# Performance work log

Measured on AMD Instinct MI355X. Metric: run time of the kernel, lower is better.

The kernel has to match this reference:

```python
import jax, jax.numpy as jnp
import numpy as np

BLOCK_SIZE = 64
NUM_STEPS = 3
# pad_type='post', init_type='ones', attention_mask=None


def setup_inputs() -> dict:
    key = jax.random.key(0)
    k1, k2, k3 = jax.random.split(key, 3)
    B, H, S, D = 4, 16, 4096, 64
    return {
        "query": jax.random.normal(k1, (B, H, S, D), dtype=jnp.float32),
        "key": jax.random.normal(k2, (B, H, S, D), dtype=jnp.float32),
        "value": jax.random.normal(k3, (B, H, S, D), dtype=jnp.float32),
    }


def _soba_monarch(query, key, value):
    B, H, S, D = query.shape
    bs = BLOCK_SIZE
    nb = -(-S // bs)                 # ceil(S / bs)
    pad = nb * bs - S                # post padding amount
    q = query / (D ** 0.5)

    pad_cfg = ((0, 0), (0, 0), (0, pad), (0, 0))
    Qb = jnp.pad(q, pad_cfg).reshape(B, H, nb, bs, D)      # (l j) v -> l j v
    Kb = jnp.pad(key, pad_cfg).reshape(B, H, nb, bs, D)    # (k i) v -> k i v

    # validity of positions in the padded sequence (post-pad)
    pos_valid = (jnp.arange(nb * bs) < S).reshape(nb, bs)  # [block, within]
    # left factor shape (..., j, l, k): rows of the flattened (l j) axis
    left_mask = jnp.broadcast_to(pos_valid.T[:, :, None], (bs, nb, nb))      # j l k
    # right factor shape (..., k, j, i): columns of the flattened (k i) axis
    right_mask = jnp.broadcast_to(pos_valid[:, None, :], (nb, bs, bs))       # k j i

    NEG = jnp.finfo(q.dtype).min
    # init_type = 'ones'
    left = jnp.broadcast_to(
        jnp.where(left_mask, 1.0 / nb, 0.0), (B, H, bs, nb, nb)
    ).astype(q.dtype)

    for _ in range(NUM_STEPS):
        # beta[k,j,i] = sum_{l,v} left[j,l,k] Q[l,j,v] K[k,i,v]
        beta = jnp.einsum('bhjlk,bhljv,bhkiv->bhkji', left, Qb, Kb, optimize=True)
        tau = jnp.swapaxes(jnp.sum(left, axis=-2), -1, -2)[..., None]        # bhkj1
        tau_zero = jnp.isclose(tau, 0.0)
        tau_safe = jnp.where(tau_zero, 1.0, tau)
        logits_r = jnp.where(right_mask & ~tau_zero, beta / tau_safe, NEG)
        right = jax.nn.softmax(logits_r, axis=-1)
        right = jnp.where(right_mask, right, 0.0)

        # alpha[j,1,k] = sum_i right[k,j,i] log right[k,j,i]  (xlogy)
        r_safe = jnp.where(right > 0, right, 1.0)
        alpha = jnp.sum(right * jnp.log(r_safe), axis=-1)                    # bhkj
        alpha = jnp.swapaxes(alpha, -1, -2)[..., None, :]                    # bhj1k

        beta2 = jnp.einsum('bhkji,bhljv,bhkiv->bhjlk', right, Qb, Kb, optimize=True)
        left = jax.nn.softmax(jnp.where(left_mask, beta2 - alpha, NEG), axis=-1)
        left = jnp.where(left_mask, left, 0.0)

    # multiply: z = L (R V)
    Vb = jnp.pad(value, pad_cfg).reshape(B, H, nb, bs, D)                    # k i v
    Y = jnp.einsum('bhkji,bhkiv->bhkjv', right, Vb)
    Z = jnp.einsum('bhjlk,bhkjv->bhljv', left, Y)
    z = Z.reshape(B, H, nb * bs, D)
    return z[..., :S, :]


def reference(query, key, value):
    return _soba_monarch(query, key, value)
```

## Files before the change

kernel.cpp:

```cpp
#include <hip/hip_runtime.h>


namespace {

typedef __attribute__((ext_vector_type(8))) short short8v;
typedef __attribute__((ext_vector_type(4))) float f32x4;

constexpr int HEADS = 64;
constexpr size_t HEADQ = 262144;
constexpr size_t MATF  = (size_t)HEADS * 262144;

#define MFMA(ACC, A, B) ACC = __builtin_amdgcn_mfma_f32_16x16x32_bf16(A, B, ACC, 0, 0, 0)
#define LD8(arr, row, g8) (*(const short8v*)((arr) + (row) * 72 + (g8) * 8))

__device__ __forceinline__ float rmax16(float m) {
    m = fmaxf(m, __shfl_xor(m, 1));
    m = fmaxf(m, __shfl_xor(m, 2));
    m = fmaxf(m, __shfl_xor(m, 4));
    m = fmaxf(m, __shfl_xor(m, 8));
    return m;
}
__device__ __forceinline__ float rsum16(float s) {
    s += __shfl_xor(s, 1);
    s += __shfl_xor(s, 2);
    s += __shfl_xor(s, 4);
    s += __shfl_xor(s, 8);
    return s;
}

__device__ __forceinline__ void bfsplit(float x, ushort& h, ushort& l) {
    uint u = __float_as_uint(x);
    uint hi = (u + 0x7FFFu + ((u >> 16) & 1u)) & 0xFFFF0000u;
    h = (ushort)(hi >> 16);
    l = (ushort)(__float_as_uint(x - __uint_as_float(hi)) >> 16);
}
__device__ __forceinline__ uint packbf(float x) {
    uint u = __float_as_uint(x);
    uint hi = (u + 0x7FFFu + ((u >> 16) & 1u)) & 0xFFFF0000u;
    return hi | (__float_as_uint(x - __uint_as_float(hi)) >> 16);
}

struct Frag16 { short8v h0, h1, l0, l1; };

__device__ __forceinline__ Frag16 load_packed16(const uint* p) {
    Frag16 f;
    #pragma unroll
    for (int q = 0; q < 4; ++q) {
        uint4 a = *(const uint4*)(p + 4 * q);
        uint vv[4] = {a.x, a.y, a.z, a.w};
        #pragma unroll
        for (int e = 0; e < 4; ++e) {
            const int i = 4 * q + e;
            const ushort hh = (ushort)(vv[e] >> 16), ll = (ushort)(vv[e] & 0xFFFFu);
            if (i < 8) { f.h0[i] = (short)hh; f.l0[i] = (short)ll; }
            else       { f.h1[i - 8] = (short)hh; f.l1[i - 8] = (short)ll; }
        }
    }
    return f;
}
__device__ __forceinline__ Frag16 load_f32x16(const float* p, float s) {
    Frag16 f;
    #pragma unroll
    for (int q = 0; q < 4; ++q) {
        float4 a = *(const float4*)(p + 4 * q);
        float vv[4] = {a.x * s, a.y * s, a.z * s, a.w * s};
        #pragma unroll
        for (int e = 0; e < 4; ++e) {
            const int i = 4 * q + e;
            ushort hh, ll; bfsplit(vv[e], hh, ll);
            if (i < 8) { f.h0[i] = (short)hh; f.l0[i] = (short)ll; }
            else       { f.h1[i - 8] = (short)hh; f.l1[i - 8] = (short)ll; }
        }
    }
    return f;
}
__device__ __forceinline__ void store_rows(ushort* H, ushort* L, int r, int c0,
                                           const Frag16& f) {
    *(short8v*)(H + r * 72 + c0)     = f.h0;
    *(short8v*)(H + r * 72 + c0 + 8) = f.h1;
    *(short8v*)(L + r * 72 + c0)     = f.l0;
    *(short8v*)(L + r * 72 + c0 + 8) = f.l1;
}
__device__ __forceinline__ void scatter_tr(ushort* H, ushort* L, int r, int c0,
                                           const Frag16& f) {
    #pragma unroll
    for (int e = 0; e < 8; ++e) {
        H[(c0 + e) * 72 + r] = (ushort)f.h0[e];
        L[(c0 + e) * 72 + r] = (ushort)f.l0[e];
    }
    #pragma unroll
    for (int e = 0; e < 8; ++e) {
        H[(c0 + 8 + e) * 72 + r] = (ushort)f.h1[e];
        L[(c0 + 8 + e) * 72 + r] = (ushort)f.l1[e];
    }
}

__device__ __forceinline__ void flush_u32(const uint* OS, uint* g, int tid) {
    #pragma unroll
    for (int q = 0; q < 4; ++q) {
        const int off = tid * 4 + q * 1024;
        uint4 v = *(const uint4*)(OS + (off >> 6) * 68 + (off & 63));
        *(uint4*)(g + off) = v;
    }
}

__device__ __forceinline__ void mmstep(const ushort* AH, const ushort* AL,
                                       const ushort* BH, const ushort* BL,
                                       int w, int lo4, int hi4, f32x4 acc[4]) {
    #pragma unroll
    for (int ks = 0; ks < 2; ++ks) {
        short8v ah = LD8(AH, 16 * w + lo4, hi4 + 4 * ks);
        short8v al = LD8(AL, 16 * w + lo4, hi4 + 4 * ks);
        #pragma unroll
        for (int t = 0; t < 4; ++t) {
            short8v bh = LD8(BH, 16 * t + lo4, hi4 + 4 * ks);
            short8v bl = LD8(BL, 16 * t + lo4, hi4 + 4 * ks);
            MFMA(acc[t], ah, bh); MFMA(acc[t], ah, bl); MFMA(acc[t], al, bh);
        }
    }
}

__global__ void kmean_kernel(const float* __restrict__ Q, uint* __restrict__ M) {
    const int wg = blockIdx.x;
    const int h  = wg >> 6, j = wg & 63;
    const int v  = threadIdx.x;
    const float* base = Q + (size_t)h * HEADQ + (size_t)j * 64 + v;
    float acc = 0.f;
    #pragma unroll
    for (int l = 0; l < 64; ++l) acc += base[(size_t)l * 4096];
    M[(size_t)wg * 64 + v] = packbf(acc * (1.0f / 512.0f));
}

template<int FIRST, int LAST>
__global__ __launch_bounds__(256) void bc_kernel(
    const uint*  __restrict__ Gsrc,
    const float* __restrict__ Kmat,
    const float* __restrict__ Vmat,
    const float* __restrict__ tauIn,
    uint*  __restrict__ HmOut,
    float* __restrict__ alphaOut,
    uint*  __restrict__ Yout)
{
    __shared__ uint SM[9216];
    ushort* Ah = (ushort*)SM;        ushort* Al = Ah + 4608;
    ushort* Bh = (ushort*)(SM + 4608); ushort* Bl = Bh + 4608;
    uint* OS  = SM + 4608;
    uint* OS2 = SM;

    const int wg = blockIdx.x, h = wg >> 6, k = wg & 63;
    const int tid = threadIdx.x, r = tid & 63, c0 = (tid >> 6) << 4;

    {
        const uint* gp = FIRST ? (Gsrc + ((size_t)h * 64 + r) * 64 + c0)
                               : (Gsrc + ((size_t)h * 64 + r) * 4096 + (size_t)k * 64 + c0);
        Frag16 fg = load_packed16(gp);
        store_rows(Ah, Al, r, c0, fg);
    }
    Frag16 fk = load_f32x16(Kmat + (size_t)h * HEADQ + (size_t)k * 4096 + r * 64 + c0, 1.f);
    store_rows(Bh, Bl, r, c0, fk);
    Frag16 fv;
    if (LAST)
        fv = load_f32x16(Vmat + (size_t)h * HEADQ + (size_t)k * 4096 + r * 64 + c0, 1.f);

    const int w = tid >> 6, lo4 = tid & 15, hi4 = (tid >> 4) & 3;
    float tvv[4];
    #pragma unroll
    for (int rr = 0; rr < 4; ++rr)
        tvv[rr] = FIRST ? 1.f : tauIn[((size_t)h * 64 + k) * 64 + 16 * w + 4 * hi4 + rr];
    __syncthreads();

    f32x4 acc[4] = {};
    mmstep(Ah, Al, Bh, Bl, w, lo4, hi4, acc);
    __syncthreads();

    #pragma unroll
    for (int rr = 0; rr < 4; ++rr) {
        const int j = 16 * w + 4 * hi4 + rr;
        const bool tz = !(tvv[rr] > 1e-8f);
        const float tvi = tz ? 1.f : 1.f / tvv[rr];
        float lg[4];
        #pragma unroll
        for (int t = 0; t < 4; ++t) lg[t] = acc[t][rr] * tvi;
        float m = rmax16(fmaxf(fmaxf(lg[0], lg[1]), fmaxf(lg[2], lg[3])));
        float e[4], s = 0.f;
        #pragma unroll
        for (int t = 0; t < 4; ++t) { e[t] = __expf(lg[t] - m); s += e[t]; }
        s = rsum16(s);
        const float inv = 1.f / s;
        float ap = 0.f;
        #pragma unroll
        for (int t = 0; t < 4; ++t) {
            const float rv = tz ? (1.f / 64.f) : e[t] * inv;
            ap += (rv > 0.f) ? rv * __logf(rv) : 0.f;
            ushort hh, ll; bfsplit(rv, hh, ll);
            Ah[j * 72 + 16 * t + lo4] = hh;
            Al[j * 72 + 16 * t + lo4] = ll;
        }
        ap = rsum16(ap);
        if (lo4 == 0) alphaOut[((size_t)h * 64 + j) * 64 + k] = ap;
    }
    scatter_tr(Bh, Bl, r, c0, fk);
    __syncthreads();

    f32x4 acc2[4] = {};
    mmstep(Ah, Al, Bh, Bl, w, lo4, hi4, acc2);
    f32x4 acc3[4] = {};
    if (LAST) {
        __syncthreads();
        scatter_tr(Bh, Bl, r, c0, fv);
        __syncthreads();
        mmstep(Ah, Al, Bh, Bl, w, lo4, hi4, acc3);
    }
    __syncthreads();

    #pragma unroll
    for (int rr = 0; rr < 4; ++rr) {
        const int j = 16 * w + 4 * hi4 + rr;
        #pragma unroll
        for (int t = 0; t < 4; ++t) OS[j * 68 + 16 * t + lo4] = packbf(acc2[t][rr]);
    }
    if (LAST) {
        #pragma unroll
        for (int rr = 0; rr < 4; ++rr) {
            const int j = 16 * w + 4 * hi4 + rr;
            #pragma unroll
            for (int t = 0; t < 4; ++t) OS2[j * 68 + 16 * t + lo4] = packbf(acc3[t][rr]);
        }
    }
    __syncthreads();
    flush_u32(OS, HmOut + (size_t)wg * 4096, tid);
    if (LAST) flush_u32(OS2, Yout + (size_t)wg * 4096, tid);
}

template<int LAST>
__global__ __launch_bounds__(256) void da_kernel(
    const float* __restrict__ Q,
    const uint*  __restrict__ HmIn,
    const float* __restrict__ alphaIn,
    const uint*  __restrict__ Yin,
    uint*  __restrict__ Gout,
    float* __restrict__ tauOut,
    float* __restrict__ Zout)
{
    __shared__ uint SM[9216];
    ushort* Ah = (ushort*)SM;        ushort* Al = Ah + 4608;
    ushort* Bh = (ushort*)(SM + 4608); ushort* Bl = Bh + 4608;
    uint*  OSu = SM + 4608;
    float* OSf = (float*)(SM + 4608);

    const int wg = blockIdx.x, h = wg >> 6, j = wg & 63;
    const int tid = threadIdx.x, r = tid & 63, c0 = (tid >> 6) << 4;

    Frag16 fq = load_f32x16(Q + (size_t)h * HEADQ + (size_t)r * 4096 + (size_t)j * 64 + c0,
                            0.125f);
    store_rows(Ah, Al, r, c0, fq);
    {
        Frag16 fh = load_packed16(HmIn + ((size_t)h * 64 + r) * 4096 + (size_t)j * 64 + c0);
        store_rows(Bh, Bl, r, c0, fh);
    }
    Frag16 fy;
    if (LAST)
        fy = load_packed16(Yin + ((size_t)h * 64 + r) * 4096 + (size_t)j * 64 + c0);

    const int w = tid >> 6, lo4 = tid & 15, hi4 = (tid >> 4) & 3;
    float av[4];
    #pragma unroll
    for (int t = 0; t < 4; ++t)
        av[t] = alphaIn[((size_t)h * 64 + j) * 64 + 16 * t + lo4];
    __syncthreads();

    f32x4 acc[4] = {};
    mmstep(Ah, Al, Bh, Bl, w, lo4, hi4, acc);
    __syncthreads();

    #pragma unroll
    for (int rr = 0; rr < 4; ++rr) {
        const int l = 16 * w + 4 * hi4 + rr;
        float lg[4];
        #pragma unroll
        for (int t = 0; t < 4; ++t) lg[t] = acc[t][rr] - av[t];
        float m = rmax16(fmaxf(fmaxf(lg[0], lg[1]), fmaxf(lg[2], lg[3])));
        float e[4], s = 0.f;
        #pragma unroll
        for (int t = 0; t < 4; ++t) { e[t] = __expf(lg[t] - m); s += e[t]; }
        s = rsum16(s);
        const float inv = 1.f / s;
        #pragma unroll
        for (int t = 0; t < 4; ++t) {
            const float lv = e[t] * inv;
            ushort hh, ll; bfsplit(lv, hh, ll);
            if (!LAST) { Bh[(16 * t + lo4) * 72 + l] = hh; Bl[(16 * t + lo4) * 72 + l] = ll; }
            else       { Bh[l * 72 + 16 * t + lo4] = hh; Bl[l * 72 + 16 * t + lo4] = ll; }
        }
    }
    if (!LAST) scatter_tr(Ah, Al, r, c0, fq);
    else       scatter_tr(Ah, Al, r, c0, fy);
    __syncthreads();

    if (!LAST) {
        f32x4 acc2[4] = {};
        f32x4 tacc = {};
        short8v onesb;
        #pragma unroll
        for (int e2 = 0; e2 < 8; ++e2) onesb[e2] = (lo4 == 0) ? (short)0x3F80 : (short)0;
        #pragma unroll
        for (int ks = 0; ks < 2; ++ks) {
            short8v ah = LD8(Bh, 16 * w + lo4, hi4 + 4 * ks);
            short8v al = LD8(Bl, 16 * w + lo4, hi4 + 4 * ks);
            MFMA(tacc, ah, onesb); MFMA(tacc, al, onesb);
            #pragma unroll
            for (int t = 0; t < 4; ++t) {
                short8v bh = LD8(Ah, 16 * t + lo4, hi4 + 4 * ks);
                short8v bl = LD8(Al, 16 * t + lo4, hi4 + 4 * ks);
                MFMA(acc2[t], ah, bh); MFMA(acc2[t], ah, bl); MFMA(acc2[t], al, bh);
            }
        }
        __syncthreads();
        #pragma unroll
        for (int rr = 0; rr < 4; ++rr) {
            const int kq = 16 * w + 4 * hi4 + rr;
            if (lo4 == 0) tauOut[((size_t)h * 64 + kq) * 64 + j] = tacc[rr];
            #pragma unroll
            for (int t = 0; t < 4; ++t) OSu[kq * 68 + 16 * t + lo4] = packbf(acc2[t][rr]);
        }
        __syncthreads();
        flush_u32(OSu, Gout + (size_t)wg * 4096, tid);
    } else {
        f32x4 acc2[4] = {};
        #pragma unroll
        for (int ks = 0; ks < 2; ++ks) {
            short8v ah = LD8(Bh, 16 * w + lo4, hi4 + 4 * ks);
            short8v al = LD8(Bl, 16 * w + lo4, hi4 + 4 * ks);
            #pragma unroll
            for (int t = 0; t < 4; ++t) {
                short8v bh = LD8(Ah, 16 * t + lo4, hi4 + 4 * ks);
                short8v bl = LD8(Al, 16 * t + lo4, hi4 + 4 * ks);
                MFMA(acc2[t], ah, bh); MFMA(acc2[t], ah, bl); MFMA(acc2[t], al, bh);
            }
        }
        __syncthreads();
        #pragma unroll
        for (int rr = 0; rr < 4; ++rr) {
            const int l = 16 * w + 4 * hi4 + rr;
            #pragma unroll
            for (int t = 0; t < 4; ++t) OSf[l * 68 + 16 * t + lo4] = acc2[t][rr];
        }
        __syncthreads();
        #pragma unroll
        for (int q = 0; q < 4; ++q) {
            const int l = (tid >> 4) + 16 * q;
            const int v4 = (tid & 15) * 4;
            float4 vv = *(const float4*)(OSf + l * 68 + v4);
            *(float4*)(Zout + (size_t)h * HEADQ + (size_t)l * 4096 + (size_t)j * 64 + v4) = vv;
        }
    }
}

}

extern "C" void kernel_launch(void* const* d_in, const int* in_sizes, int n_in,
                              void* d_out, int out_size, void* d_ws, size_t ws_size,
                              hipStream_t stream) {
    const float* Q = (const float*)d_in[0];
    const float* K = (const float*)d_in[1];
    const float* V = (const float*)d_in[2];
    float* out = (float*)d_out;

    char* ws = (char*)d_ws;
    const size_t MB = 1024 * 1024;
    uint*  G   = (uint*)(ws);
    uint*  Hm  = (uint*)(ws + 64 * MB);
    uint*  M   = (uint*)(ws + 128 * MB);
    float* al  = (float*)(ws + 129 * MB);
    float* tau = (float*)(ws + 130 * MB);

    const bool bigws = ws_size >= (size_t)196 * MB;
    uint*  Ybuf = bigws ? (uint*)(ws + 131 * MB) : (uint*)out;
    float* Zdst = bigws ? out : (float*)G;

    dim3 blk(256), grid(HEADS * 64);

    kmean_kernel<<<dim3(HEADS * 64), dim3(64), 0, stream>>>(Q, M);
    bc_kernel<1, 0><<<grid, blk, 0, stream>>>(M, K, nullptr, nullptr, Hm, al, nullptr);
    da_kernel<0>   <<<grid, blk, 0, stream>>>(Q, Hm, al, nullptr, G, tau, nullptr);
    bc_kernel<0, 0><<<grid, blk, 0, stream>>>(G, K, nullptr, tau, Hm, al, nullptr);
    da_kernel<0>   <<<grid, blk, 0, stream>>>(Q, Hm, al, nullptr, G, tau, nullptr);
    bc_kernel<0, 1><<<grid, blk, 0, stream>>>(G, K, V, tau, Hm, al, Ybuf);
    da_kernel<1>   <<<grid, blk, 0, stream>>>(Q, Hm, al, Ybuf, nullptr, nullptr, Zdst);
    if (!bigws)
        hipMemcpyAsync(d_out, G, MATF * sizeof(float), hipMemcpyDeviceToDevice, stream);
}
```

Baseline: 305.5 us.

## Swizzle LDS tiles and store intermediates as separate hi/lo bf16 planes

Replaces the padded 72-stride LDS layout with an XOR-swizzled 64-stride layout so fragment loads avoid bank conflicts while using less shared memory. Intermediate matrices (G, Hm, Y, kmean) are stored as separate high and low bf16 planes instead of packed uint, so loads become direct vector copies with no unpacking. kmean is widened to 256 threads, and launch bounds request 5 blocks per CU for higher occupancy. This adds a fallback path for the small-workspace case, and the swizzle adds index arithmetic on scattered LDS stores.

```diff
diff --git a/kernel.cpp b/kernel.cpp
--- a/kernel.cpp
+++ b/kernel.cpp
@@ -11,7 +11,13 @@
 constexpr size_t MATF  = (size_t)HEADS * 262144;
 
 #define MFMA(ACC, A, B) ACC = __builtin_amdgcn_mfma_f32_16x16x32_bf16(A, B, ACC, 0, 0, 0)
-#define LD8(arr, row, g8) (*(const short8v*)((arr) + (row) * 72 + (g8) * 8))
+
+__device__ __forceinline__ int swz(int row, int col) {
+    return row * 64 + (((col >> 3) ^ (row & 7)) << 3) + (col & 7);
+}
+__device__ __forceinline__ short8v ldx(const ushort* a, int row, int chunk) {
+    return *(const short8v*)(a + row * 64 + ((chunk ^ (row & 7)) << 3));
+}
 
 __device__ __forceinline__ float rmax16(float m) {
     m = fmaxf(m, __shfl_xor(m, 1));
@@ -34,74 +40,57 @@
     h = (ushort)(hi >> 16);
     l = (ushort)(__float_as_uint(x - __uint_as_float(hi)) >> 16);
 }
-__device__ __forceinline__ uint packbf(float x) {
-    uint u = __float_as_uint(x);
-    uint hi = (u + 0x7FFFu + ((u >> 16) & 1u)) & 0xFFFF0000u;
-    return hi | (__float_as_uint(x - __uint_as_float(hi)) >> 16);
-}
 
 struct Frag16 { short8v h0, h1, l0, l1; };
 
-__device__ __forceinline__ Frag16 load_packed16(const uint* p) {
+__device__ __forceinline__ Frag16 split_load(const float* __restrict__ p, float s) {
     Frag16 f;
     #pragma unroll
     for (int q = 0; q < 4; ++q) {
-        uint4 a = *(const uint4*)(p + 4 * q);
-        uint vv[4] = {a.x, a.y, a.z, a.w};
+        float4 a = *(const float4*)(p + 4 * q);
+        float v[4] = {a.x * s, a.y * s, a.z * s, a.w * s};
         #pragma unroll
         for (int e = 0; e < 4; ++e) {
+            ushort hh, ll; bfsplit(v[e], hh, ll);
             const int i = 4 * q + e;
-            const ushort hh = (ushort)(vv[e] >> 16), ll = (ushort)(vv[e] & 0xFFFFu);
             if (i < 8) { f.h0[i] = (short)hh; f.l0[i] = (short)ll; }
             else       { f.h1[i - 8] = (short)hh; f.l1[i - 8] = (short)ll; }
         }
     }
     return f;
 }
-__device__ __forceinline__ Frag16 load_f32x16(const float* p, float s) {
+__device__ __forceinline__ Frag16 copy_load(const ushort* __restrict__ gh,
+                                            const ushort* __restrict__ gl) {
     Frag16 f;
-    #pragma unroll
-    for (int q = 0; q < 4; ++q) {
-        float4 a = *(const float4*)(p + 4 * q);
-        float vv[4] = {a.x * s, a.y * s, a.z * s, a.w * s};
-        #pragma unroll
-        for (int e = 0; e < 4; ++e) {
-            const int i = 4 * q + e;
-            ushort hh, ll; bfsplit(vv[e], hh, ll);
-            if (i < 8) { f.h0[i] = (short)hh; f.l0[i] = (short)ll; }
-            else       { f.h1[i - 8] = (short)hh; f.l1[i - 8] = (short)ll; }
-        }
-    }
+    f.h0 = *(const short8v*)(gh);     f.h1 = *(const short8v*)(gh + 8);
+    f.l0 = *(const short8v*)(gl);     f.l1 = *(const short8v*)(gl + 8);
     return f;
 }
 __device__ __forceinline__ void store_rows(ushort* H, ushort* L, int r, int c0,
                                            const Frag16& f) {
-    *(short8v*)(H + r * 72 + c0)     = f.h0;
-    *(short8v*)(H + r * 72 + c0 + 8) = f.h1;
-    *(short8v*)(L + r * 72 + c0)     = f.l0;
-    *(short8v*)(L + r * 72 + c0 + 8) = f.l1;
+    const int ch = c0 >> 3;
+    const int o0 = r * 64 + ((ch ^ (r & 7)) << 3);
+    const int o1 = r * 64 + (((ch + 1) ^ (r & 7)) << 3);
+    *(short8v*)(H + o0) = f.h0; *(short8v*)(H + o1) = f.h1;
+    *(short8v*)(L + o0) = f.l0; *(short8v*)(L + o1) = f.l1;
 }
 __device__ __forceinline__ void scatter_tr(ushort* H, ushort* L, int r, int c0,
                                            const Frag16& f) {
     #pragma unroll
     for (int e = 0; e < 8; ++e) {
-        H[(c0 + e) * 72 + r] = (ushort)f.h0[e];
-        L[(c0 + e) * 72 + r] = (ushort)f.l0[e];
+        H[swz(c0 + e, r)] = (ushort)f.h0[e];
+        L[swz(c0 + e, r)] = (ushort)f.l0[e];
     }
     #pragma unroll
     for (int e = 0; e < 8; ++e) {
-        H[(c0 + 8 + e) * 72 + r] = (ushort)f.h1[e];
-        L[(c0 + 8 + e) * 72 + r] = (ushort)f.l1[e];
-    }
-}
-
-__device__ __forceinline__ void flush_u32(const uint* OS, uint* g, int tid) {
-    #pragma unroll
-    for (int q = 0; q < 4; ++q) {
-        const int off = tid * 4 + q * 1024;
-        uint4 v = *(const uint4*)(OS + (off >> 6) * 68 + (off & 63));
-        *(uint4*)(g + off) = v;
-    }
+        H[swz(c0 + 8 + e, r)] = (ushort)f.h1[e];
+        L[swz(c0 + 8 + e, r)] = (ushort)f.l1[e];
+    }
+}
+
+__device__ __forceinline__ void flush_u16(const ushort* OS, ushort* g, int tid) {
+    *(short8v*)(g + tid * 16)     = *(const short8v*)(OS + tid * 16);
+    *(short8v*)(g + tid * 16 + 8) = *(const short8v*)(OS + tid * 16 + 8);
 }
 
 __device__ __forceinline__ void mmstep(const ushort* AH, const ushort* AL,
@@ -109,60 +98,65 @@
                                        int w, int lo4, int hi4, f32x4 acc[4]) {
     #pragma unroll
     for (int ks = 0; ks < 2; ++ks) {
-        short8v ah = LD8(AH, 16 * w + lo4, hi4 + 4 * ks);
-        short8v al = LD8(AL, 16 * w + lo4, hi4 + 4 * ks);
+        short8v ah = ldx(AH, 16 * w + lo4, hi4 + 4 * ks);
+        short8v al = ldx(AL, 16 * w + lo4, hi4 + 4 * ks);
         #pragma unroll
         for (int t = 0; t < 4; ++t) {
-            short8v bh = LD8(BH, 16 * t + lo4, hi4 + 4 * ks);
-            short8v bl = LD8(BL, 16 * t + lo4, hi4 + 4 * ks);
+            short8v bh = ldx(BH, 16 * t + lo4, hi4 + 4 * ks);
+            short8v bl = ldx(BL, 16 * t + lo4, hi4 + 4 * ks);
             MFMA(acc[t], ah, bh); MFMA(acc[t], ah, bl); MFMA(acc[t], al, bh);
         }
     }
 }
 
-__global__ void kmean_kernel(const float* __restrict__ Q, uint* __restrict__ M) {
+__global__ __launch_bounds__(256) void kmean_kernel(const float* __restrict__ Q,
+                                                    ushort* __restrict__ Mh,
+                                                    ushort* __restrict__ Ml) {
     const int wg = blockIdx.x;
-    const int h  = wg >> 6, j = wg & 63;
-    const int v  = threadIdx.x;
+    const int h  = wg >> 4;
+    const int j  = ((wg & 15) << 2) + (threadIdx.x >> 6);
+    const int v  = threadIdx.x & 63;
     const float* base = Q + (size_t)h * HEADQ + (size_t)j * 64 + v;
     float acc = 0.f;
     #pragma unroll
     for (int l = 0; l < 64; ++l) acc += base[(size_t)l * 4096];
-    M[(size_t)wg * 64 + v] = packbf(acc * (1.0f / 512.0f));
-}
-
-template<int FIRST, int LAST>
-__global__ __launch_bounds__(256) void bc_kernel(
-    const uint*  __restrict__ Gsrc,
-    const float* __restrict__ Kmat,
-    const float* __restrict__ Vmat,
-    const float* __restrict__ tauIn,
-    uint*  __restrict__ HmOut,
-    float* __restrict__ alphaOut,
-    uint*  __restrict__ Yout)
+    ushort hh, ll; bfsplit(acc * (1.0f / 512.0f), hh, ll);
+    Mh[((size_t)h * 64 + j) * 64 + v] = hh;
+    Ml[((size_t)h * 64 + j) * 64 + v] = ll;
+}
+
+template<int FIRST, int LAST, int YSPLIT>
+__global__ __launch_bounds__(256, 5) void bc_kernel(
+    const ushort* __restrict__ Gsh,
+    const ushort* __restrict__ Gsl,
+    const float*  __restrict__ Kmat,
+    const float*  __restrict__ Vmat,
+    const float*  __restrict__ tauIn,
+    ushort* __restrict__ Hmh,
+    ushort* __restrict__ Hml,
+    float*  __restrict__ alphaOut,
+    ushort* __restrict__ Yh,
+    ushort* __restrict__ Yl,
+    float*  __restrict__ Yf)
 {
-    __shared__ uint SM[9216];
-    ushort* Ah = (ushort*)SM;        ushort* Al = Ah + 4608;
-    ushort* Bh = (ushort*)(SM + 4608); ushort* Bl = Bh + 4608;
-    uint* OS  = SM + 4608;
-    uint* OS2 = SM;
+    __shared__ __align__(16) ushort SM[16384];
+    ushort* Ah = SM;          ushort* Al = SM + 4096;
+    ushort* Bh = SM + 8192;   ushort* Bl = SM + 12288;
 
     const int wg = blockIdx.x, h = wg >> 6, k = wg & 63;
     const int tid = threadIdx.x, r = tid & 63, c0 = (tid >> 6) << 4;
+    const int w = tid >> 6, lo4 = tid & 15, hi4 = (tid >> 4) & 3;
 
     {
-        const uint* gp = FIRST ? (Gsrc + ((size_t)h * 64 + r) * 64 + c0)
-                               : (Gsrc + ((size_t)h * 64 + r) * 4096 + (size_t)k * 64 + c0);
-        Frag16 fg = load_packed16(gp);
-        store_rows(Ah, Al, r, c0, fg);
-    }
-    Frag16 fk = load_f32x16(Kmat + (size_t)h * HEADQ + (size_t)k * 4096 + r * 64 + c0, 1.f);
+        const size_t gb = FIRST ? (((size_t)h * 64 + r) * 64 + c0)
+                                : (((size_t)h * 64 + r) * 4096 + (size_t)k * 64 + c0);
+        store_rows(Ah, Al, r, c0, copy_load(Gsh + gb, Gsl + gb));
+    }
+    Frag16 fk = split_load(Kmat + (size_t)h * HEADQ + (size_t)k * 4096 + r * 64 + c0, 1.f);
     store_rows(Bh, Bl, r, c0, fk);
     Frag16 fv;
     if (LAST)
-        fv = load_f32x16(Vmat + (size_t)h * HEADQ + (size_t)k * 4096 + r * 64 + c0, 1.f);
-
-    const int w = tid >> 6, lo4 = tid & 15, hi4 = (tid >> 4) & 3;
+        fv = split_load(Vmat + (size_t)h * HEADQ + (size_t)k * 4096 + r * 64 + c0, 1.f);
     float tvv[4];
     #pragma unroll
     for (int rr = 0; rr < 4; ++rr)
@@ -193,8 +187,8 @@
             const float rv = tz ? (1.f / 64.f) : e[t] * inv;
             ap += (rv > 0.f) ? rv * __logf(rv) : 0.f;
             ushort hh, ll; bfsplit(rv, hh, ll);
-            Ah[j * 72 + 16 * t + lo4] = hh;
-            Al[j * 72 + 16 * t + lo4] = ll;
+            const int idx = swz(j, 16 * t + lo4);
+            Ah[idx] = hh; Al[idx] = ll;
         }
         ap = rsum16(ap);
         if (lo4 == 0) alphaOut[((size_t)h * 64 + j) * 64 + k] = ap;
@@ -217,52 +211,73 @@
     for (int rr = 0; rr < 4; ++rr) {
         const int j = 16 * w + 4 * hi4 + rr;
         #pragma unroll
-        for (int t = 0; t < 4; ++t) OS[j * 68 + 16 * t + lo4] = packbf(acc2[t][rr]);
-    }
+        for (int t = 0; t < 4; ++t) {
+            ushort hh, ll; bfsplit(acc2[t][rr], hh, ll);
+            Bh[j * 64 + 16 * t + lo4] = hh;
+            Bl[j * 64 + 16 * t + lo4] = ll;
+            if (LAST) {
+                if (YSPLIT) {
+                    ushort yh, yl; bfsplit(acc3[t][rr], yh, yl);
+                    Ah[j * 64 + 16 * t + lo4] = yh;
+                    Al[j * 64 + 16 * t + lo4] = yl;
+                } else {
+                    ((float*)Ah)[j * 64 + 16 * t + lo4] = acc3[t][rr];
+                }
+            }
+        }
+    }
+    __syncthreads();
+    const size_t ob = ((size_t)h * 64 + k) * 4096;
+    flush_u16(Bh, Hmh + ob, tid);
+    flush_u16(Bl, Hml + ob, tid);
     if (LAST) {
-        #pragma unroll
-        for (int rr = 0; rr < 4; ++rr) {
-            const int j = 16 * w + 4 * hi4 + rr;
+        if (YSPLIT) {
+            flush_u16(Ah, Yh + ob, tid);
+            flush_u16(Al, Yl + ob, tid);
+        } else {
+            const float* Zs = (const float*)Ah;
             #pragma unroll
-            for (int t = 0; t < 4; ++t) OS2[j * 68 + 16 * t + lo4] = packbf(acc3[t][rr]);
-        }
-    }
-    __syncthreads();
-    flush_u32(OS, HmOut + (size_t)wg * 4096, tid);
-    if (LAST) flush_u32(OS2, Yout + (size_t)wg * 4096, tid);
-}
-
-template<int LAST>
-__global__ __launch_bounds__(256) void da_kernel(
-    const float* __restrict__ Q,
-    const uint*  __restrict__ HmIn,
-    const float* __restrict__ alphaIn,
-    const uint*  __restrict__ Yin,
-    uint*  __restrict__ Gout,
-    float* __restrict__ tauOut,
-    float* __restrict__ Zout)
+            for (int q = 0; q < 4; ++q)
+                *(float4*)(Yf + ob + tid * 16 + 4 * q) = *(const float4*)(Zs + tid * 16 + 4 * q);
+        }
+    }
+}
+
+template<int LAST, int YSPLIT>
+__global__ __launch_bounds__(256, 5) void da_kernel(
+    const float*  __restrict__ Q,
+    const ushort* __restrict__ Hmh,
+    const ushort* __restrict__ Hml,
+    const float*  __restrict__ alphaIn,
+    const ushort* __restrict__ Yh,
+    const ushort* __restrict__ Yl,
+    const float*  __restrict__ Yf,
+    ushort* __restrict__ Goh,
+    ushort* __restrict__ Gol,
+    float*  __restrict__ tauOut,
+    float*  __restrict__ Zout)
 {
-    __shared__ uint SM[9216];
-    ushort* Ah = (ushort*)SM;        ushort* Al = Ah + 4608;
-    ushort* Bh = (ushort*)(SM + 4608); ushort* Bl = Bh + 4608;
-    uint*  OSu = SM + 4608;
-    float* OSf = (float*)(SM + 4608);
+    __shared__ __align__(16) ushort SM[16384];
+    ushort* Ah = SM;          ushort* Al = SM + 4096;
+    ushort* Bh = SM + 8192;   ushort* Bl = SM + 12288;
 
     const int wg = blockIdx.x, h = wg >> 6, j = wg & 63;
     const int tid = threadIdx.x, r = tid & 63, c0 = (tid >> 6) << 4;
-
-    Frag16 fq = load_f32x16(Q + (size_t)h * HEADQ + (size_t)r * 4096 + (size_t)j * 64 + c0,
-                            0.125f);
+    const int w = tid >> 6, lo4 = tid & 15, hi4 = (tid >> 4) & 3;
+
+    Frag16 fq = split_load(Q + (size_t)h * HEADQ + (size_t)r * 4096 + (size_t)j * 64 + c0,
+                           0.125f);
     store_rows(Ah, Al, r, c0, fq);
     {
-        Frag16 fh = load_packed16(HmIn + ((size_t)h * 64 + r) * 4096 + (size_t)j * 64 + c0);
-        store_rows(Bh, Bl, r, c0, fh);
+        const size_t hb = ((size_t)h * 64 + r) * 4096 + (size_t)j * 64 + c0;
+        store_rows(Bh, Bl, r, c0, copy_load(Hmh + hb, Hml + hb));
     }
     Frag16 fy;
-    if (LAST)
-        fy = load_packed16(Yin + ((size_t)h * 64 + r) * 4096 + (size_t)j * 64 + c0);
-
-    const int w = tid >> 6, lo4 = tid & 15, hi4 = (tid >> 4) & 3;
+    if (LAST) {
+        const size_t yb = ((size_t)h * 64 + r) * 4096 + (size_t)j * 64 + c0;
+        if (YSPLIT) fy = copy_load(Yh + yb, Yl + yb);
+        else        fy = split_load(Yf + yb, 1.f);
+    }
     float av[4];
     #pragma unroll
     for (int t = 0; t < 4; ++t)
@@ -289,8 +304,8 @@
         for (int t = 0; t < 4; ++t) {
             const float lv = e[t] * inv;
             ushort hh, ll; bfsplit(lv, hh, ll);
-            if (!LAST) { Bh[(16 * t + lo4) * 72 + l] = hh; Bl[(16 * t + lo4) * 72 + l] = ll; }
-            else       { Bh[l * 72 + 16 * t + lo4] = hh; Bl[l * 72 + 16 * t + lo4] = ll; }
+            const int idx = LAST ? swz(l, 16 * t + lo4) : swz(16 * t + lo4, l);
+            Bh[idx] = hh; Bl[idx] = ll;
         }
     }
     if (!LAST) scatter_tr(Ah, Al, r, c0, fq);
@@ -305,13 +320,13 @@
         for (int e2 = 0; e2 < 8; ++e2) onesb[e2] = (lo4 == 0) ? (short)0x3F80 : (short)0;
         #pragma unroll
         for (int ks = 0; ks < 2; ++ks) {
-            short8v ah = LD8(Bh, 16 * w + lo4, hi4 + 4 * ks);
-            short8v al = LD8(Bl, 16 * w + lo4, hi4 + 4 * ks);
+            short8v ah = ldx(Bh, 16 * w + lo4, hi4 + 4 * ks);
+            short8v al = ldx(Bl, 16 * w + lo4, hi4 + 4 * ks);
             MFMA(tacc, ah, onesb); MFMA(tacc, al, onesb);
             #pragma unroll
             for (int t = 0; t < 4; ++t) {
-                short8v bh = LD8(Ah, 16 * t + lo4, hi4 + 4 * ks);
-                short8v bl = LD8(Al, 16 * t + lo4, hi4 + 4 * ks);
+                short8v bh = ldx(Ah, 16 * t + lo4, hi4 + 4 * ks);
+                short8v bl = ldx(Al, 16 * t + lo4, hi4 + 4 * ks);
                 MFMA(acc2[t], ah, bh); MFMA(acc2[t], ah, bl); MFMA(acc2[t], al, bh);
             }
         }
@@ -321,36 +336,43 @@
             const int kq = 16 * w + 4 * hi4 + rr;
             if (lo4 == 0) tauOut[((size_t)h * 64 + kq) * 64 + j] = tacc[rr];
             #pragma unroll
-            for (int t = 0; t < 4; ++t) OSu[kq * 68 + 16 * t + lo4] = packbf(acc2[t][rr]);
-        }
-        __syncthreads();
-        flush_u32(OSu, Gout + (size_t)wg * 4096, tid);
+            for (int t = 0; t < 4; ++t) {
+                ushort hh, ll; bfsplit(acc2[t][rr], hh, ll);
+                Bh[kq * 64 + 16 * t + lo4] = hh;
+                Bl[kq * 64 + 16 * t + lo4] = ll;
+            }
+        }
+        __syncthreads();
+        const size_t ob = ((size_t)h * 64 + j) * 4096;
+        flush_u16(Bh, Goh + ob, tid);
+        flush_u16(Bl, Gol + ob, tid);
     } else {
         f32x4 acc2[4] = {};
         #pragma unroll
         for (int ks = 0; ks < 2; ++ks) {
-            short8v ah = LD8(Bh, 16 * w + lo4, hi4 + 4 * ks);
-            short8v al = LD8(Bl, 16 * w + lo4, hi4 + 4 * ks);
+            short8v ah = ldx(Bh, 16 * w + lo4, hi4 + 4 * ks);
+            short8v al = ldx(Bl, 16 * w + lo4, hi4 + 4 * ks);
             #pragma unroll
             for (int t = 0; t < 4; ++t) {
-                short8v bh = LD8(Ah, 16 * t + lo4, hi4 + 4 * ks);
-                short8v bl = LD8(Al, 16 * t + lo4, hi4 + 4 * ks);
+                short8v bh = ldx(Ah, 16 * t + lo4, hi4 + 4 * ks);
+                short8v bl = ldx(Al, 16 * t + lo4, hi4 + 4 * ks);
                 MFMA(acc2[t], ah, bh); MFMA(acc2[t], ah, bl); MFMA(acc2[t], al, bh);
             }
         }
         __syncthreads();
+        float* Zs = (float*)Ah;
         #pragma unroll
         for (int rr = 0; rr < 4; ++rr) {
             const int l = 16 * w + 4 * hi4 + rr;
             #pragma unroll
-            for (int t = 0; t < 4; ++t) OSf[l * 68 + 16 * t + lo4] = acc2[t][rr];
+            for (int t = 0; t < 4; ++t) Zs[l * 64 + 16 * t + lo4] = acc2[t][rr];
         }
         __syncthreads();
         #pragma unroll
         for (int q = 0; q < 4; ++q) {
             const int l = (tid >> 4) + 16 * q;
             const int v4 = (tid & 15) * 4;
-            float4 vv = *(const float4*)(OSf + l * 68 + v4);
+            float4 vv = *(const float4*)(Zs + l * 64 + v4);
             *(float4*)(Zout + (size_t)h * HEADQ + (size_t)l * 4096 + (size_t)j * 64 + v4) = vv;
         }
     }
@@ -368,25 +390,42 @@
 
     char* ws = (char*)d_ws;
     const size_t MB = 1024 * 1024;
-    uint*  G   = (uint*)(ws);
-    uint*  Hm  = (uint*)(ws + 64 * MB);
-    uint*  M   = (uint*)(ws + 128 * MB);
-    float* al  = (float*)(ws + 129 * MB);
-    float* tau = (float*)(ws + 130 * MB);
-
-    const bool bigws = ws_size >= (size_t)196 * MB;
-    uint*  Ybuf = bigws ? (uint*)(ws + 131 * MB) : (uint*)out;
-    float* Zdst = bigws ? out : (float*)G;
+    ushort* Gh  = (ushort*)(ws);
+    ushort* Gl  = (ushort*)(ws + 32 * MB);
+    ushort* Hmh = (ushort*)(ws + 64 * MB);
+    ushort* Hml = (ushort*)(ws + 96 * MB);
+    ushort* Mh  = (ushort*)(ws + 128 * MB);
+    ushort* Ml  = (ushort*)(ws + 128 * MB + 512 * 1024);
+    float*  al  = (float*)(ws + 129 * MB);
+    float*  tau = (float*)(ws + 130 * MB);
+
+    const bool bigws = ws_size >= (size_t)195 * MB;
+    ushort* Yh = bigws ? (ushort*)(ws + 131 * MB) : nullptr;
+    ushort* Yl = bigws ? (ushort*)(ws + 163 * MB) : nullptr;
+    float*  Yf = bigws ? nullptr : out;
+    float*  Zdst = bigws ? out : (float*)ws;
 
     dim3 blk(256), grid(HEADS * 64);
 
-    kmean_kernel<<<dim3(HEADS * 64), dim3(64), 0, stream>>>(Q, M);
-    bc_kernel<1, 0><<<grid, blk, 0, stream>>>(M, K, nullptr, nullptr, Hm, al, nullptr);
-    da_kernel<0>   <<<grid, blk, 0, stream>>>(Q, Hm, al, nullptr, G, tau, nullptr);
-    bc_kernel<0, 0><<<grid, blk, 0, stream>>>(G, K, nullptr, tau, Hm, al, nullptr);
-    da_kernel<0>   <<<grid, blk, 0, stream>>>(Q, Hm, al, nullptr, G, tau, nullptr);
-    bc_kernel<0, 1><<<grid, blk, 0, stream>>>(G, K, V, tau, Hm, al, Ybuf);
-    da_kernel<1>   <<<grid, blk, 0, stream>>>(Q, Hm, al, Ybuf, nullptr, nullptr, Zdst);
-    if (!bigws)
-        hipMemcpyAsync(d_out, G, MATF * sizeof(float), hipMemcpyDeviceToDevice, stream);
-}
+    kmean_kernel<<<dim3(1024), blk, 0, stream>>>(Q, Mh, Ml);
+    bc_kernel<1, 0, 0><<<grid, blk, 0, stream>>>(Mh, Ml, K, nullptr, nullptr,
+                                                 Hmh, Hml, al, nullptr, nullptr, nullptr);
+    da_kernel<0, 0>   <<<grid, blk, 0, stream>>>(Q, Hmh, Hml, al, nullptr, nullptr, nullptr,
+                                                 Gh, Gl, tau, nullptr);
+    bc_kernel<0, 0, 0><<<grid, blk, 0, stream>>>(Gh, Gl, K, nullptr, tau,
+                                                 Hmh, Hml, al, nullptr, nullptr, nullptr);
+    da_kernel<0, 0>   <<<grid, blk, 0, stream>>>(Q, Hmh, Hml, al, nullptr, nullptr, nullptr,
+                                                 Gh, Gl, tau, nullptr);
+    if (bigws) {
+        bc_kernel<0, 1, 1><<<grid, blk, 0, stream>>>(Gh, Gl, K, V, tau,
+                                                     Hmh, Hml, al, Yh, Yl, nullptr);
+        da_kernel<1, 1>   <<<grid, blk, 0, stream>>>(Q, Hmh, Hml, al, Yh, Yl, nullptr,
+                                                     nullptr, nullptr, nullptr, Zdst);
+    } else {
+        bc_kernel<0, 1, 0><<<grid, blk, 0, stream>>>(Gh, Gl, K, V, tau,
+                                                     Hmh, Hml, al, nullptr, nullptr, Yf);
+        da_kernel<1, 0>   <<<grid, blk, 0, stream>>>(Q, Hmh, Hml, al, nullptr, nullptr, Yf,
+                                                     nullptr, nullptr, nullptr, Zdst);
+        hipMemcpyAsync(d_out, Zdst, MATF * sizeof(float), hipMemcpyDeviceToDevice, stream);
+    }
+}
```

New measurement: 373.6 us. 1.22x slower.

## Write outputs directly to global, transpose alpha/tau layouts, widen kmean blocks

Applied to the files above, without the earlier changes.

Removes the LDS staging buffers and extra barriers at the end of the bc and da kernels, so results are stored straight from MFMA accumulators to global memory with 16-lane coalesced scalar stores. The alpha and tau buffers switch to transposed layouts so the writes and reads line up differently. The kmean kernel moves to 256-thread blocks, and the other kernels get occupancy hints through launch_bounds. The trade-off is narrower, less coalesced global stores in exchange for fewer syncs and less shared-memory traffic.

```diff
diff --git a/kernel.cpp b/kernel.cpp
--- a/kernel.cpp
+++ b/kernel.cpp
@@ -42,35 +42,36 @@
 
 struct Frag16 { short8v h0, h1, l0, l1; };
 
-__device__ __forceinline__ Frag16 load_packed16(const uint* p) {
+__device__ __forceinline__ Frag16 split_load(const float* __restrict__ p, float s) {
     Frag16 f;
     #pragma unroll
     for (int q = 0; q < 4; ++q) {
-        uint4 a = *(const uint4*)(p + 4 * q);
-        uint vv[4] = {a.x, a.y, a.z, a.w};
+        float4 a = *(const float4*)(p + 4 * q);
+        float v[4] = {a.x * s, a.y * s, a.z * s, a.w * s};
         #pragma unroll
         for (int e = 0; e < 4; ++e) {
+            ushort hh, ll; bfsplit(v[e], hh, ll);
             const int i = 4 * q + e;
-            const ushort hh = (ushort)(vv[e] >> 16), ll = (ushort)(vv[e] & 0xFFFFu);
             if (i < 8) { f.h0[i] = (short)hh; f.l0[i] = (short)ll; }
             else       { f.h1[i - 8] = (short)hh; f.l1[i - 8] = (short)ll; }
         }
     }
     return f;
 }
-__device__ __forceinline__ Frag16 load_f32x16(const float* p, float s) {
+__device__ __forceinline__ Frag16 unpack_load(const uint* __restrict__ p) {
     Frag16 f;
     #pragma unroll
-    for (int q = 0; q < 4; ++q) {
-        float4 a = *(const float4*)(p + 4 * q);
-        float vv[4] = {a.x * s, a.y * s, a.z * s, a.w * s};
-        #pragma unroll
-        for (int e = 0; e < 4; ++e) {
-            const int i = 4 * q + e;
-            ushort hh, ll; bfsplit(vv[e], hh, ll);
-            if (i < 8) { f.h0[i] = (short)hh; f.l0[i] = (short)ll; }
-            else       { f.h1[i - 8] = (short)hh; f.l1[i - 8] = (short)ll; }
-        }
+    for (int q = 0; q < 2; ++q) {
+        uint4 a = *(const uint4*)(p + 8 * q);
+        uint4 b = *(const uint4*)(p + 8 * q + 4);
+        uint vv[8] = {a.x, a.y, a.z, a.w, b.x, b.y, b.z, b.w};
+        short8v h, l;
+        #pragma unroll
+        for (int e = 0; e < 8; ++e) {
+            h[e] = (short)(vv[e] >> 16);
+            l[e] = (short)(vv[e] & 0xFFFFu);
+        }
+        if (q == 0) { f.h0 = h; f.l0 = l; } else { f.h1 = h; f.l1 = l; }
     }
     return f;
 }
@@ -95,15 +96,6 @@
     }
 }
 
-__device__ __forceinline__ void flush_u32(const uint* OS, uint* g, int tid) {
-    #pragma unroll
-    for (int q = 0; q < 4; ++q) {
-        const int off = tid * 4 + q * 1024;
-        uint4 v = *(const uint4*)(OS + (off >> 6) * 68 + (off & 63));
-        *(uint4*)(g + off) = v;
-    }
-}
-
 __device__ __forceinline__ void mmstep(const ushort* AH, const ushort* AL,
                                        const ushort* BH, const ushort* BL,
                                        int w, int lo4, int hi4, f32x4 acc[4]) {
@@ -120,19 +112,21 @@
     }
 }
 
-__global__ void kmean_kernel(const float* __restrict__ Q, uint* __restrict__ M) {
+__global__ __launch_bounds__(256) void kmean_kernel(const float* __restrict__ Q,
+                                                    uint* __restrict__ M) {
     const int wg = blockIdx.x;
-    const int h  = wg >> 6, j = wg & 63;
-    const int v  = threadIdx.x;
+    const int h  = wg >> 4;
+    const int j  = ((wg & 15) << 2) + (threadIdx.x >> 6);
+    const int v  = threadIdx.x & 63;
     const float* base = Q + (size_t)h * HEADQ + (size_t)j * 64 + v;
     float acc = 0.f;
     #pragma unroll
     for (int l = 0; l < 64; ++l) acc += base[(size_t)l * 4096];
-    M[(size_t)wg * 64 + v] = packbf(acc * (1.0f / 512.0f));
+    M[((size_t)h * 64 + j) * 64 + v] = packbf(acc * (1.0f / 512.0f));
 }
 
 template<int FIRST, int LAST>
-__global__ __launch_bounds__(256) void bc_kernel(
+__global__ __launch_bounds__(256, 4) void bc_kernel(
     const uint*  __restrict__ Gsrc,
     const float* __restrict__ Kmat,
     const float* __restrict__ Vmat,
@@ -141,32 +135,28 @@
     float* __restrict__ alphaOut,
     uint*  __restrict__ Yout)
 {
-    __shared__ uint SM[9216];
-    ushort* Ah = (ushort*)SM;        ushort* Al = Ah + 4608;
-    ushort* Bh = (ushort*)(SM + 4608); ushort* Bl = Bh + 4608;
-    uint* OS  = SM + 4608;
-    uint* OS2 = SM;
+    __shared__ __align__(16) ushort SM[18432];
+    ushort* Ah = SM;          ushort* Al = SM + 4608;
+    ushort* Bh = SM + 9216;   ushort* Bl = SM + 13824;
 
     const int wg = blockIdx.x, h = wg >> 6, k = wg & 63;
     const int tid = threadIdx.x, r = tid & 63, c0 = (tid >> 6) << 4;
+    const int w = tid >> 6, lo4 = tid & 15, hi4 = (tid >> 4) & 3;
 
     {
-        const uint* gp = FIRST ? (Gsrc + ((size_t)h * 64 + r) * 64 + c0)
-                               : (Gsrc + ((size_t)h * 64 + r) * 4096 + (size_t)k * 64 + c0);
-        Frag16 fg = load_packed16(gp);
-        store_rows(Ah, Al, r, c0, fg);
-    }
-    Frag16 fk = load_f32x16(Kmat + (size_t)h * HEADQ + (size_t)k * 4096 + r * 64 + c0, 1.f);
+        const uint* gp = FIRST ? Gsrc + ((size_t)h * 64 + r) * 64 + c0
+                               : Gsrc + ((size_t)h * 64 + r) * 4096 + (size_t)k * 64 + c0;
+        store_rows(Ah, Al, r, c0, unpack_load(gp));
+    }
+    Frag16 fk = split_load(Kmat + (size_t)h * HEADQ + (size_t)k * 4096 + r * 64 + c0, 1.f);
     store_rows(Bh, Bl, r, c0, fk);
     Frag16 fv;
     if (LAST)
-        fv = load_f32x16(Vmat + (size_t)h * HEADQ + (size_t)k * 4096 + r * 64 + c0, 1.f);
-
-    const int w = tid >> 6, lo4 = tid & 15, hi4 = (tid >> 4) & 3;
+        fv = split_load(Vmat + (size_t)h * HEADQ + (size_t)k * 4096 + r * 64 + c0, 1.f);
     float tvv[4];
     #pragma unroll
     for (int rr = 0; rr < 4; ++rr)
-        tvv[rr] = FIRST ? 1.f : tauIn[((size_t)h * 64 + k) * 64 + 16 * w + 4 * hi4 + rr];
+        tvv[rr] = FIRST ? 1.f : tauIn[((size_t)h * 64 + 16 * w + 4 * hi4 + rr) * 64 + k];
     __syncthreads();
 
     f32x4 acc[4] = {};
@@ -197,7 +187,7 @@
             Al[j * 72 + 16 * t + lo4] = ll;
         }
         ap = rsum16(ap);
-        if (lo4 == 0) alphaOut[((size_t)h * 64 + j) * 64 + k] = ap;
+        if (lo4 == 0) alphaOut[((size_t)h * 64 + k) * 64 + j] = ap;
     }
     scatter_tr(Bh, Bl, r, c0, fk);
     __syncthreads();
@@ -211,29 +201,21 @@
         __syncthreads();
         mmstep(Ah, Al, Bh, Bl, w, lo4, hi4, acc3);
     }
-    __syncthreads();
 
     #pragma unroll
     for (int rr = 0; rr < 4; ++rr) {
         const int j = 16 * w + 4 * hi4 + rr;
-        #pragma unroll
-        for (int t = 0; t < 4; ++t) OS[j * 68 + 16 * t + lo4] = packbf(acc2[t][rr]);
-    }
-    if (LAST) {
-        #pragma unroll
-        for (int rr = 0; rr < 4; ++rr) {
-            const int j = 16 * w + 4 * hi4 + rr;
-            #pragma unroll
-            for (int t = 0; t < 4; ++t) OS2[j * 68 + 16 * t + lo4] = packbf(acc3[t][rr]);
-        }
-    }
-    __syncthreads();
-    flush_u32(OS, HmOut + (size_t)wg * 4096, tid);
-    if (LAST) flush_u32(OS2, Yout + (size_t)wg * 4096, tid);
+        const size_t ob = ((size_t)h * 64 + k) * 4096 + (size_t)j * 64;
+        #pragma unroll
+        for (int t = 0; t < 4; ++t) {
+            HmOut[ob + 16 * t + lo4] = packbf(acc2[t][rr]);
+            if (LAST) Yout[ob + 16 * t + lo4] = packbf(acc3[t][rr]);
+        }
+    }
 }
 
 template<int LAST>
-__global__ __launch_bounds__(256) void da_kernel(
+__global__ __launch_bounds__(256, 4) void da_kernel(
     const float* __restrict__ Q,
     const uint*  __restrict__ HmIn,
     const float* __restrict__ alphaIn,
@@ -242,31 +224,28 @@
     float* __restrict__ tauOut,
     float* __restrict__ Zout)
 {
-    __shared__ uint SM[9216];
-    ushort* Ah = (ushort*)SM;        ushort* Al = Ah + 4608;
-    ushort* Bh = (ushort*)(SM + 4608); ushort* Bl = Bh + 4608;
-    uint*  OSu = SM + 4608;
-    float* OSf = (float*)(SM + 4608);
+    __shared__ __align__(16) ushort SM[18432];
+    ushort* Ah = SM;          ushort* Al = SM + 4608;
+    ushort* Bh = SM + 9216;   ushort* Bl = SM + 13824;
 
     const int wg = blockIdx.x, h = wg >> 6, j = wg & 63;
     const int tid = threadIdx.x, r = tid & 63, c0 = (tid >> 6) << 4;
-
-    Frag16 fq = load_f32x16(Q + (size_t)h * HEADQ + (size_t)r * 4096 + (size_t)j * 64 + c0,
-                            0.125f);
+    const int w = tid >> 6, lo4 = tid & 15, hi4 = (tid >> 4) & 3;
+
+    Frag16 fq = split_load(Q + (size_t)h * HEADQ + (size_t)r * 4096 + (size_t)j * 64 + c0,
+                           0.125f);
     store_rows(Ah, Al, r, c0, fq);
     {
-        Frag16 fh = load_packed16(HmIn + ((size_t)h * 64 + r) * 4096 + (size_t)j * 64 + c0);
-        store_rows(Bh, Bl, r, c0, fh);
+        store_rows(Bh, Bl, r, c0,
+                   unpack_load(HmIn + ((size_t)h * 64 + r) * 4096 + (size_t)j * 64 + c0));
     }
     Frag16 fy;
     if (LAST)
-        fy = load_packed16(Yin + ((size_t)h * 64 + r) * 4096 + (size_t)j * 64 + c0);
-
-    const int w = tid >> 6, lo4 = tid & 15, hi4 = (tid >> 4) & 3;
+        fy = unpack_load(Yin + ((size_t)h * 64 + r) * 4096 + (size_t)j * 64 + c0);
     float av[4];
     #pragma unroll
     for (int t = 0; t < 4; ++t)
-        av[t] = alphaIn[((size_t)h * 64 + j) * 64 + 16 * t + lo4];
+        av[t] = alphaIn[((size_t)h * 64 + 16 * t + lo4) * 64 + j];
     __syncthreads();
 
     f32x4 acc[4] = {};
@@ -315,16 +294,14 @@
                 MFMA(acc2[t], ah, bh); MFMA(acc2[t], ah, bl); MFMA(acc2[t], al, bh);
             }
         }
-        __syncthreads();
         #pragma unroll
         for (int rr = 0; rr < 4; ++rr) {
             const int kq = 16 * w + 4 * hi4 + rr;
-            if (lo4 == 0) tauOut[((size_t)h * 64 + kq) * 64 + j] = tacc[rr];
+            if (lo4 == 0) tauOut[((size_t)h * 64 + j) * 64 + kq] = tacc[rr];
+            const size_t gb = ((size_t)h * 64 + j) * 4096 + (size_t)kq * 64;
             #pragma unroll
-            for (int t = 0; t < 4; ++t) OSu[kq * 68 + 16 * t + lo4] = packbf(acc2[t][rr]);
-        }
-        __syncthreads();
-        flush_u32(OSu, Gout + (size_t)wg * 4096, tid);
+            for (int t = 0; t < 4; ++t) Gout[gb + 16 * t + lo4] = packbf(acc2[t][rr]);
+        }
     } else {
         f32x4 acc2[4] = {};
         #pragma unroll
@@ -338,20 +315,12 @@
                 MFMA(acc2[t], ah, bh); MFMA(acc2[t], ah, bl); MFMA(acc2[t], al, bh);
             }
         }
-        __syncthreads();
         #pragma unroll
         for (int rr = 0; rr < 4; ++rr) {
             const int l = 16 * w + 4 * hi4 + rr;
+            const size_t zb = (size_t)h * HEADQ + (size_t)l * 4096 + (size_t)j * 64;
             #pragma unroll
-            for (int t = 0; t < 4; ++t) OSf[l * 68 + 16 * t + lo4] = acc2[t][rr];
-        }
-        __syncthreads();
-        #pragma unroll
-        for (int q = 0; q < 4; ++q) {
-            const int l = (tid >> 4) + 16 * q;
-            const int v4 = (tid & 15) * 4;
-            float4 vv = *(const float4*)(OSf + l * 68 + v4);
-            *(float4*)(Zout + (size_t)h * HEADQ + (size_t)l * 4096 + (size_t)j * 64 + v4) = vv;
+            for (int t = 0; t < 4; ++t) Zout[zb + 16 * t + lo4] = acc2[t][rr];
         }
     }
 }
@@ -374,13 +343,13 @@
     float* al  = (float*)(ws + 129 * MB);
     float* tau = (float*)(ws + 130 * MB);
 
-    const bool bigws = ws_size >= (size_t)196 * MB;
+    const bool bigws = ws_size >= (size_t)195 * MB;
     uint*  Ybuf = bigws ? (uint*)(ws + 131 * MB) : (uint*)out;
     float* Zdst = bigws ? out : (float*)G;
 
     dim3 blk(256), grid(HEADS * 64);
 
-    kmean_kernel<<<dim3(HEADS * 64), dim3(64), 0, stream>>>(Q, M);
+    kmean_kernel<<<dim3(1024), blk, 0, stream>>>(Q, M);
     bc_kernel<1, 0><<<grid, blk, 0, stream>>>(M, K, nullptr, nullptr, Hm, al, nullptr);
     da_kernel<0>   <<<grid, blk, 0, stream>>>(Q, Hm, al, nullptr, G, tau, nullptr);
     bc_kernel<0, 0><<<grid, blk, 0, stream>>>(G, K, nullptr, tau, Hm, al, nullptr);
@@ -388,5 +357,5 @@
     bc_kernel<0, 1><<<grid, blk, 0, stream>>>(G, K, V, tau, Hm, al, Ybuf);
     da_kernel<1>   <<<grid, blk, 0, stream>>>(Q, Hm, al, Ybuf, nullptr, nullptr, Zdst);
     if (!bigws)
-        hipMemcpyAsync(d_out, G, MATF * sizeof(float), hipMemcpyDeviceToDevice, stream);
-}
+        hipMemcpyAsync(d_out, Zdst, MATF * sizeof(float), hipMemcpyDeviceToDevice, stream);
+}
```

After: 328.9 us. 1.08x slower.
